# Performance work log

Measured on AMD Instinct MI355X. Metric: run time of the kernel, lower is better.

Reference implementation:

```python
import jax, jax.numpy as jnp
import numpy as np

VOCAB, HID = 32000, 1024
SEQ, BATCH = 64, 32

def setup_inputs() -> dict:
    key = jax.random.key(0)
    ks = jax.random.split(key, 12)
    w = 0.1  # winit uniform(-winit, winit)
    u = lambda k, shape: jax.random.uniform(k, shape, jnp.float32, -w, w)
    return {
        "x": jax.random.randint(ks[0], (SEQ, BATCH), 0, VOCAB),
        "emb_W": u(ks[1], (VOCAB, HID)),
        "Wx0": u(ks[2], (4 * HID, HID)), "Wh0": u(ks[3], (4 * HID, HID)),
        "bx0": u(ks[4], (4 * HID,)), "bh0": u(ks[5], (4 * HID,)),
        "Wx1": u(ks[6], (4 * HID, HID)), "Wh1": u(ks[7], (4 * HID, HID)),
        "bx1": u(ks[8], (4 * HID,)), "bh1": u(ks[9], (4 * HID,)),
        "fc_W": u(ks[10], (VOCAB, HID)), "fc_b": u(ks[11], (VOCAB,)),
        "h0": jnp.zeros((BATCH, HID), jnp.float32),
        "c0": jnp.zeros((BATCH, HID), jnp.float32),
        "h1": jnp.zeros((BATCH, HID), jnp.float32),
        "c1": jnp.zeros((BATCH, HID), jnp.float32),
    }

def _lstm_layer(inp, h, c, Wx, Wh, bx, bh):
    # inp: [T, B, H]; h, c: [B, H]
    def step(carry, x_t):
        h, c = carry
        gx = x_t @ Wx.T + bx      # [B, 4H]
        gh = h @ Wh.T + bh        # [B, 4H]
        xi, xf, xo, xn = jnp.split(gx, 4, axis=1)
        hi, hf, ho, hn = jnp.split(gh, 4, axis=1)
        i = jax.nn.sigmoid(xi + hi)
        f = jax.nn.sigmoid(xf + hf)
        o = jax.nn.sigmoid(xo + ho)
        n = jnp.tanh(xn + hn)
        c = f * c + i * n
        h = o * jnp.tanh(c)
        return (h, c), h
    (h, c), ys = jax.lax.scan(step, (h, c), inp)
    return ys, h, c

def reference(x, emb_W, Wx0, Wh0, bx0, bh0, Wx1, Wh1, bx1, bh1,
              fc_W, fc_b, h0, c0, h1, c1):
    e = emb_W[x]                                   # [T, B, H] embedding gather
    y0, h0f, c0f = _lstm_layer(e, h0, c0, Wx0, Wh0, bx0, bh0)
    y1, h1f, c1f = _lstm_layer(y0, h1, c1, Wx1, Wh1, bx1, bh1)
    # Linear.forward flattens to [T*B, H] then projects to vocab (dropout=0)
    logits = y1.reshape(-1, y1.shape[-1]) @ fc_W.T + fc_b  # [T*B, V]
    return logits, h0f, c0f, h1f, c1f
```

## Files before the change

kernel.cpp:

```cpp
#include <hip/hip_runtime.h>
#include <hip/hip_bf16.h>
#include <stdint.h>

typedef __bf16 bf16x8 __attribute__((ext_vector_type(8)));
typedef float  f32x4  __attribute__((ext_vector_type(4)));

#define HID   1024
#define SEQT  64
#define BATCH 32
#define GATES 4096
#define ROWS  2048
#define VOCAB 32000
#define HSLAB (64 * 32 * 16)
#define AGT __HIP_MEMORY_SCOPE_AGENT

__device__ __forceinline__ unsigned short f2bf(float f) {
    union { float f; unsigned u; } v; v.f = f;
    unsigned u = v.u + 0x7FFFu + ((v.u >> 16) & 1u);
    return (unsigned short)(u >> 16);
}

__device__ __forceinline__ float sigm(float x) { return 1.f / (1.f + expf(-x)); }

__device__ __forceinline__ void gload_lds16(const void* g, void* l) {
    __builtin_amdgcn_global_load_lds(
        (const __attribute__((address_space(1))) unsigned int*)g,
        (__attribute__((address_space(3))) unsigned int*)l,
        16, 0, 0);
}

__device__ __forceinline__ ushort4 cvt4(float4 v) {
    ushort4 o;
    o.x = f2bf(v.x); o.y = f2bf(v.y); o.z = f2bf(v.z); o.w = f2bf(v.w);
    return o;
}

__global__ __launch_bounds__(256) void prologue_k(
    const int* __restrict__ x, const float* __restrict__ embW,
    unsigned short* __restrict__ eb,
    const float* __restrict__ Wx0, unsigned short* __restrict__ Wx0b,
    const float* __restrict__ h0, const float* __restrict__ h1,
    unsigned short* __restrict__ h0b, unsigned short* __restrict__ h1b,
    int* __restrict__ bar)
{
    const int bid = blockIdx.x, tid = threadIdx.x;
    const float4* src = (const float4*)(embW + (size_t)x[bid] * HID);
    ((ushort4*)(eb + (size_t)bid * HID))[tid] = cvt4(src[tid]);
    int base = bid * 512 + tid;
    ((ushort4*)Wx0b)[base]       = cvt4(((const float4*)Wx0)[base]);
    ((ushort4*)Wx0b)[base + 256] = cvt4(((const float4*)Wx0)[base + 256]);
    int i = bid * 256 + tid;
    if (i < 32768) {
        int blk = i >> 9, b = (i >> 4) & 31, w = i & 15;
        int col = blk * 16 + w;
        h0b[i] = f2bf(h0[b * HID + col]);
        h1b[i] = f2bf(h1[b * HID + col]);
        if (i < 8192) bar[i] = 0;
    }
}

__global__ __launch_bounds__(256) void gemm_bt(
    const unsigned short* __restrict__ A,
    const unsigned short* __restrict__ B,
    float* __restrict__ C,
    const float* __restrict__ bias0,
    const float* __restrict__ bias1,
    int M, int N, int K)
{
    __shared__ unsigned short As[128][32];
    __shared__ unsigned short Bs[128][32];
    const int tid  = threadIdx.x;
    const int lane = tid & 63;
    const int wr   = (tid >> 7) & 1;
    const int wc   = (tid >> 6) & 1;

    const int nmp = M >> 7, nnp = N >> 7;
    const int nwg = nmp * nnp, per = nwg >> 3;
    const int wid = (blockIdx.x & 7) * per + (blockIdx.x >> 3);
    const int bm  = (wid % nmp) << 7;
    const int bn  = (wid / nmp) << 7;

    const int lr   = lane & 15;
    const int lk   = (lane >> 4) * 8;

    f32x4 acc[4][4];
    #pragma unroll
    for (int m = 0; m < 4; ++m)
        #pragma unroll
        for (int n = 0; n < 4; ++n) acc[m][n] = 0.f;

    for (int kt = 0; kt < K; kt += 32) {
        __syncthreads();
        #pragma unroll
        for (int i = 0; i < 2; ++i) {
            int ch = tid + i * 256;
            int r = ch >> 2, c8 = (ch & 3) * 8;
            gload_lds16(A + (size_t)(bm + r) * K + kt + c8, (char*)&As[0][0] + ch * 16);
            gload_lds16(B + (size_t)(bn + r) * K + kt + c8, (char*)&Bs[0][0] + ch * 16);
        }
        __syncthreads();
        bf16x8 af[4], bfr[4];
        #pragma unroll
        for (int m = 0; m < 4; ++m)
            af[m] = *(const bf16x8*)&As[wr * 64 + m * 16 + lr][lk];
        #pragma unroll
        for (int n = 0; n < 4; ++n)
            bfr[n] = *(const bf16x8*)&Bs[wc * 64 + n * 16 + lr][lk];
        #pragma unroll
        for (int m = 0; m < 4; ++m)
            #pragma unroll
            for (int n = 0; n < 4; ++n)
                acc[m][n] = __builtin_amdgcn_mfma_f32_16x16x32_bf16(af[m], bfr[n], acc[m][n], 0, 0, 0);
    }

    const int row0 = bm + wr * 64, col0 = bn + wc * 64;
    #pragma unroll
    for (int n = 0; n < 4; ++n) {
        int col = col0 + n * 16 + lr;
        float badd = 0.f;
        if (bias0) badd += bias0[col];
        if (bias1) badd += bias1[col];
        #pragma unroll
        for (int m = 0; m < 4; ++m) {
            #pragma unroll
            for (int j = 0; j < 4; ++j) {
                int row = row0 + m * 16 + (lane >> 4) * 4 + j;
                C[(size_t)row * N + col] = acc[m][n][j] + badd;
            }
        }
    }
}

__global__ __launch_bounds__(256, 1) void lstm_fused_k(
    const float* __restrict__ Wh0f,
    const float* __restrict__ Wx1f,
    const float* __restrict__ Wh1f,
    const float* __restrict__ gx0,
    const float* __restrict__ bx1,
    const float* __restrict__ bh1,
    const unsigned short* __restrict__ h0b,
    const unsigned short* __restrict__ h1b,
    const float* __restrict__ c0i,
    const float* __restrict__ c1i,
    unsigned short* __restrict__ y0x,
    unsigned short* __restrict__ y1x,
    float* __restrict__ part,
    float* __restrict__ h0f, float* __restrict__ c0f,
    float* __restrict__ h1f, float* __restrict__ c1f,
    int* __restrict__ bar,
    const float* __restrict__ fcW,
    unsigned short* __restrict__ fcWb)
{
    const int tid = threadIdx.x;
    const int bid = blockIdx.x;

    if (bid >= 192) {
        int base = (bid - 192) * 256 + tid;
        const float4* f4 = (const float4*)fcW;
        uint4* o4 = (uint4*)fcWb;
        const int n8 = VOCAB * HID / 8;
        for (int i = base; i < n8; i += 16384) {
            float4 v0 = f4[2 * i], v1 = f4[2 * i + 1];
            uint4 o;
            o.x = (unsigned)f2bf(v0.x) | ((unsigned)f2bf(v0.y) << 16);
            o.y = (unsigned)f2bf(v0.z) | ((unsigned)f2bf(v0.w) << 16);
            o.z = (unsigned)f2bf(v1.x) | ((unsigned)f2bf(v1.y) << 16);
            o.w = (unsigned)f2bf(v1.z) | ((unsigned)f2bf(v1.w) << 16);
            o4[i] = o;
        }
        return;
    }

    __builtin_amdgcn_fence(__ATOMIC_ACQUIRE, "agent");

    __shared__ char smem[65536 + 8192];
    float* pre = (float*)(smem + 65536);
    const int lane = tid & 63;
    const int wave = tid >> 6;
    const int role = bid >> 6;
    const int wg   = bid & 63;
    const int lr   = lane & 15;
    const int lk8  = (lane >> 4) * 8;
    const int r0   = lr, r1 = 16 + lr;
    const int kby  = (lane >> 4) * 16;
    const int eb_  = tid >> 3;
    const int ecp  = (tid & 7) * 2;
    const int ecol = wg * 16 + ecp;

    bf16x8 wf[32];
    {
        const float* Wsrc = (role == 0) ? Wh0f : (role == 1) ? Wx1f : Wh1f;
        const float* p = Wsrc + (size_t)(wave * HID + wg * 16 + lr) * HID + lk8;
        #pragma unroll
        for (int kk = 0; kk < 32; ++kk) {
            float4 v0 = *(const float4*)(p + kk * 32);
            float4 v1 = *(const float4*)(p + kk * 32 + 4);
            union { bf16x8 v; unsigned short s[8]; } u;
            u.s[0] = f2bf(v0.x); u.s[1] = f2bf(v0.y);
            u.s[2] = f2bf(v0.z); u.s[3] = f2bf(v0.w);
            u.s[4] = f2bf(v1.x); u.s[5] = f2bf(v1.y);
            u.s[6] = f2bf(v1.z); u.s[7] = f2bf(v1.w);
            wf[kk] = u.v;
        }
        #pragma unroll
        for (int kk = 0; kk < 32; ++kk) asm volatile("" : "+v"(wf[kk]));
    }

    auto stage_g = [&](const unsigned short* src) {
        #pragma unroll
        for (int j = 0; j < 16; ++j) {
            int base = wave * 16384 + j * 1024;
            int d = base + lane * 16;
            int r = d >> 11;
            int cb = (d & 2047) ^ ((r & 7) << 4);
            int e0 = cb >> 1;
            int g = (((e0 >> 4) * 32 + r) * 16 + (e0 & 15)) * 2;
            gload_lds16((const char*)src + g, smem + base);
        }
    };
    auto mm = [&](f32x4& A0, f32x4& A1) {
        #pragma unroll
        for (int kk = 0; kk < 32; ++kk) {
            int k2 = kk * 64 + kby;
            bf16x8 x0 = *(const bf16x8*)(smem + r0 * 2048 + (k2 ^ ((r0 & 7) << 4)));
            bf16x8 x1 = *(const bf16x8*)(smem + r1 * 2048 + (k2 ^ ((r1 & 7) << 4)));
            A0 = __builtin_amdgcn_mfma_f32_16x16x32_bf16(x0, wf[kk], A0, 0, 0, 0);
            A1 = __builtin_amdgcn_mfma_f32_16x16x32_bf16(x1, wf[kk], A1, 0, 0, 0);
        }
    };
    auto spill = [&](const f32x4& a0, const f32x4& a1) {
        float* pg = pre + wave * 512;
        #pragma unroll
        for (int j = 0; j < 4; ++j) {
            pg[((lane >> 4) * 4 + j) * 16 + lr]        = a0[j];
            pg[((lane >> 4) * 4 + j + 16) * 16 + lr]   = a1[j];
        }
    };
    auto pollge = [&](int grp, int val) {
        for (;;) {
            int f = __hip_atomic_load(&bar[(grp * 64 + lane) * 32],
                                      __ATOMIC_RELAXED, AGT);
            if (__all(f >= val)) break;
            __builtin_amdgcn_s_sleep(1);
        }
    };

    if (role == 0) {
        float creg0, creg1;
        { float2 c2 = *(const float2*)&c0i[eb_ * HID + ecol]; creg0 = c2.x; creg1 = c2.y; }
        for (int t = 0; t < SEQT; ++t) {
            float2 gpre[4];
            const float* gxr = gx0 + (size_t)(t * BATCH + eb_) * GATES + ecol;
            #pragma unroll
            for (int g = 0; g < 4; ++g) gpre[g] = *(const float2*)(gxr + g * HID);
            if (t > 0) pollge(0, t);
            asm volatile("" ::: "memory");
            stage_g(t == 0 ? h0b : y0x + (size_t)(t - 1) * HSLAB);
            __syncthreads();
            f32x4 a0 = 0.f, a1 = 0.f;
            mm(a0, a1);
            spill(a0, a1);
            __syncthreads();
            float2 P[4];
            #pragma unroll
            for (int g = 0; g < 4; ++g) {
                float2 pr = *(const float2*)&pre[(g * 32 + eb_) * 16 + ecp];
                P[g].x = pr.x + gpre[g].x; P[g].y = pr.y + gpre[g].y;
            }
            float i0 = sigm(P[0].x), fg0 = sigm(P[1].x), o0 = sigm(P[2].x), n0 = tanhf(P[3].x);
            float i1 = sigm(P[0].y), fg1 = sigm(P[1].y), o1 = sigm(P[2].y), n1 = tanhf(P[3].y);
            float cn0 = fg0 * creg0 + i0 * n0, cn1 = fg1 * creg1 + i1 * n1;
            float hv0 = o0 * tanhf(cn0), hv1 = o1 * tanhf(cn1);
            creg0 = cn0; creg1 = cn1;
            unsigned pk = (unsigned)f2bf(hv0) | ((unsigned)f2bf(hv1) << 16);
            __hip_atomic_store(
                (unsigned*)&y0x[(size_t)t * HSLAB + (wg * 32 + eb_) * 16 + ecp],
                pk, __ATOMIC_RELAXED, AGT);
            if (t == SEQT - 1) {
                *(float2*)&h0f[eb_ * HID + ecol] = make_float2(hv0, hv1);
                *(float2*)&c0f[eb_ * HID + ecol] = make_float2(cn0, cn1);
            }
            __syncthreads();
            if (tid == 0)
                __hip_atomic_store(&bar[wg * 32], t + 1, __ATOMIC_RELAXED, AGT);
        }
    } else if (role == 1) {
        for (int t = 0; t < SEQT; ++t) {
            pollge(0, t + 1);
            asm volatile("" ::: "memory");
            stage_g(y0x + (size_t)t * HSLAB);
            __syncthreads();
            f32x4 a0 = 0.f, a1 = 0.f;
            mm(a0, a1);
            {
                float* pb = part + (((size_t)(t * 4 + wave) * 64 + wg) * 32) * 16;
                int brow = (lane >> 4) * 4;
                #pragma unroll
                for (int j = 0; j < 4; ++j) {
                    __hip_atomic_store(pb + (brow + j) * 16 + lr,      a0[j],
                                       __ATOMIC_RELAXED, AGT);
                    __hip_atomic_store(pb + (brow + j + 16) * 16 + lr, a1[j],
                                       __ATOMIC_RELAXED, AGT);
                }
            }
            __syncthreads();
            if (tid == 0)
                __hip_atomic_store(&bar[(64 + wg) * 32], t + 1, __ATOMIC_RELAXED, AGT);
        }
    } else {
        float creg0, creg1;
        { float2 c2 = *(const float2*)&c1i[eb_ * HID + ecol]; creg0 = c2.x; creg1 = c2.y; }
        float2 b1r[4];
        #pragma unroll
        for (int g = 0; g < 4; ++g) {
            float2 a = *(const float2*)&bx1[g * HID + ecol];
            float2 b = *(const float2*)&bh1[g * HID + ecol];
            b1r[g].x = a.x + b.x; b1r[g].y = a.y + b.y;
        }
        for (int t = 0; t < SEQT; ++t) {
            pollge(1, t + 1);
            if (t > 0) pollge(2, t);
            asm volatile("" ::: "memory");
            stage_g(t == 0 ? h1b : y1x + (size_t)(t - 1) * HSLAB);
            __syncthreads();
            f32x4 a0 = 0.f, a1 = 0.f;
            mm(a0, a1);
            spill(a0, a1);
            __syncthreads();
            float2 P[4];
            #pragma unroll
            for (int g = 0; g < 4; ++g) {
                float2 pr = *(const float2*)&pre[(g * 32 + eb_) * 16 + ecp];
                float2 px = *(const float2*)(part +
                    ((((size_t)(t * 4 + g) * 64 + wg) * 32 + eb_) * 16 + ecp));
                P[g].x = pr.x + px.x + b1r[g].x;
                P[g].y = pr.y + px.y + b1r[g].y;
            }
            float i0 = sigm(P[0].x), fg0 = sigm(P[1].x), o0 = sigm(P[2].x), n0 = tanhf(P[3].x);
            float i1 = sigm(P[0].y), fg1 = sigm(P[1].y), o1 = sigm(P[2].y), n1 = tanhf(P[3].y);
            float cn0 = fg0 * creg0 + i0 * n0, cn1 = fg1 * creg1 + i1 * n1;
            float hv0 = o0 * tanhf(cn0), hv1 = o1 * tanhf(cn1);
            creg0 = cn0; creg1 = cn1;
            unsigned pk = (unsigned)f2bf(hv0) | ((unsigned)f2bf(hv1) << 16);
            __hip_atomic_store(
                (unsigned*)&y1x[(size_t)t * HSLAB + (wg * 32 + eb_) * 16 + ecp],
                pk, __ATOMIC_RELAXED, AGT);
            if (t == SEQT - 1) {
                *(float2*)&h1f[eb_ * HID + ecol] = make_float2(hv0, hv1);
                *(float2*)&c1f[eb_ * HID + ecol] = make_float2(cn0, cn1);
            }
            __syncthreads();
            if (tid == 0)
                __hip_atomic_store(&bar[(128 + wg) * 32], t + 1, __ATOMIC_RELAXED, AGT);
        }
    }
}

__global__ __launch_bounds__(512, 4) void fc_k(
    const unsigned short* __restrict__ y1x,
    const unsigned short* __restrict__ fcWb,
    const float* __restrict__ fcb,
    float* __restrict__ logits)
{
    __shared__ unsigned short As[256 * 32];
    __shared__ unsigned short Bs[128 * 32];
    const int tid  = threadIdx.x;
    const int lane = tid & 63;
    const int wave = tid >> 6;
    const int wr   = wave >> 1;
    const int wc   = wave & 1;
    const int lr   = lane & 15;
    const int lk   = (lane >> 4) * 8;

    const int per = 2000 >> 3;
    const int wid = ((int)blockIdx.x & 7) * per + ((int)blockIdx.x >> 3);
    const int bm  = (wid & 7) << 8;
    const int bn  = (wid >> 3) << 7;

    f32x4 acc[4][4];
    #pragma unroll
    for (int m = 0; m < 4; ++m)
        #pragma unroll
        for (int n = 0; n < 4; ++n) acc[m][n] = 0.f;

    for (int kt = 0; kt < HID; kt += 32) {
        __syncthreads();
        #pragma unroll
        for (int i = 0; i < 2; ++i) {
            int ch = tid + i * 512;
            int r = ch >> 2, c8 = (ch & 3) * 8;
            int R = bm + r, e = kt + c8;
            const char* asrc = (const char*)y1x +
                ((((size_t)(R >> 5) * 64 + (e >> 4)) * 32 + (R & 31)) * 16 + (e & 15)) * 2;
            gload_lds16(asrc, (char*)As + ch * 16);
        }
        {
            int r = tid >> 2, c8 = (tid & 3) * 8;
            gload_lds16(fcWb + (size_t)(bn + r) * HID + kt + c8, (char*)Bs + tid * 16);
        }
        __syncthreads();
        bf16x8 af[4], bfr[4];
        #pragma unroll
        for (int m = 0; m < 4; ++m)
            af[m] = *(const bf16x8*)&As[(wr * 64 + m * 16 + lr) * 32 + lk];
        #pragma unroll
        for (int n = 0; n < 4; ++n)
            bfr[n] = *(const bf16x8*)&Bs[(wc * 64 + n * 16 + lr) * 32 + lk];
        #pragma unroll
        for (int m = 0; m < 4; ++m)
            #pragma unroll
            for (int n = 0; n < 4; ++n)
                acc[m][n] = __builtin_amdgcn_mfma_f32_16x16x32_bf16(af[m], bfr[n], acc[m][n], 0, 0, 0);
    }

    const int row0 = bm + wr * 64, col0 = bn + wc * 64;
    #pragma unroll
    for (int n = 0; n < 4; ++n) {
        int col = col0 + n * 16 + lr;
        float badd = fcb[col];
        #pragma unroll
        for (int m = 0; m < 4; ++m) {
            #pragma unroll
            for (int j = 0; j < 4; ++j) {
                int row = row0 + m * 16 + (lane >> 4) * 4 + j;
                logits[(size_t)row * VOCAB + col] = acc[m][n][j] + badd;
            }
        }
    }
}

extern "C" void kernel_launch(void* const* d_in, const int* in_sizes, int n_in,
                              void* d_out, int out_size, void* d_ws, size_t ws_size,
                              hipStream_t stream) {
    const int*   x    = (const int*)d_in[0];
    const float* embW = (const float*)d_in[1];
    const float* Wx0  = (const float*)d_in[2];
    const float* Wh0  = (const float*)d_in[3];
    const float* bx0  = (const float*)d_in[4];
    const float* bh0  = (const float*)d_in[5];
    const float* Wx1  = (const float*)d_in[6];
    const float* Wh1  = (const float*)d_in[7];
    const float* bx1  = (const float*)d_in[8];
    const float* bh1  = (const float*)d_in[9];
    const float* fcW  = (const float*)d_in[10];
    const float* fcb  = (const float*)d_in[11];
    const float* h0   = (const float*)d_in[12];
    const float* c0   = (const float*)d_in[13];
    const float* h1   = (const float*)d_in[14];
    const float* c1   = (const float*)d_in[15];

    char* ws = (char*)d_ws;
    size_t off = 0;
    auto alloc = [&](size_t bytes) {
        char* p = ws + off;
        off += (bytes + 255) & ~(size_t)255;
        return p;
    };
    unsigned short* eb    = (unsigned short*)alloc((size_t)ROWS * HID * 2);
    unsigned short* Wx0b  = (unsigned short*)alloc((size_t)GATES * HID * 2);
    unsigned short* fcWb  = (unsigned short*)alloc((size_t)VOCAB * HID * 2);
    float*          gx0   = (float*)alloc((size_t)ROWS * GATES * 4);
    float*          part  = (float*)alloc((size_t)SEQT * 4 * 64 * 32 * 16 * 4);
    unsigned short* y0x   = (unsigned short*)alloc((size_t)SEQT * HSLAB * 2);
    unsigned short* y1x   = (unsigned short*)alloc((size_t)SEQT * HSLAB * 2);
    unsigned short* h0b   = (unsigned short*)alloc((size_t)BATCH * HID * 2);
    unsigned short* h1b   = (unsigned short*)alloc((size_t)BATCH * HID * 2);
    int*            bar   = (int*)alloc((size_t)256 * 32 * 4);
    (void)ws_size; (void)in_sizes; (void)n_in; (void)out_size;

    float* logits = (float*)d_out;
    float* h0f = logits + (size_t)ROWS * VOCAB;
    float* c0f = h0f + BATCH * HID;
    float* h1f = c0f + BATCH * HID;
    float* c1f = h1f + BATCH * HID;

    prologue_k<<<ROWS, 256, 0, stream>>>(x, embW, eb, Wx0, Wx0b,
                                         h0, h1, h0b, h1b, bar);
    gemm_bt<<<(ROWS / 128) * (GATES / 128), 256, 0, stream>>>(
        eb, Wx0b, gx0, bx0, bh0, ROWS, GATES, HID);
    lstm_fused_k<<<256, 256, 0, stream>>>(Wh0, Wx1, Wh1, gx0, bx1, bh1,
                                          h0b, h1b, c0, c1, y0x, y1x, part,
                                          h0f, c0f, h1f, c1f, bar, fcW, fcWb);
    fc_k<<<2000, 512, 0, stream>>>(y1x, fcWb, fcb, logits);
}
```

Measured before the change: 572.5 us.

## Replace flag barriers with NaN-sentinel polling on hidden-state slabs

Removes the per-step flag barriers and the LDS staging of hidden states. Consumers now read bf16 activations straight from global memory with atomic loads and spin until no word equals a NaN sentinel that the prologue writes into the y0/y1 buffers. Layer 1 now keeps both Wx1 and Wh1 in registers in one workgroup, which drops the separate Wx1 role and the partial-sum buffer and frees 64 blocks for the fcW conversion. This shortens the dependency chain per step, but it costs more register pressure, heavier global polling traffic, and it fails if a real hidden value ever equals the sentinel pattern.

```diff
diff --git a/kernel.cpp b/kernel.cpp
--- a/kernel.cpp
+++ b/kernel.cpp
@@ -12,6 +12,7 @@
 #define ROWS  2048
 #define VOCAB 32000
 #define HSLAB (64 * 32 * 16)
+#define SENTW 0x7FC07FC0u
 #define AGT __HIP_MEMORY_SCOPE_AGENT
 
 __device__ __forceinline__ unsigned short f2bf(float f) {
@@ -33,6 +34,13 @@
     ushort4 o;
     o.x = f2bf(v.x); o.y = f2bf(v.y); o.z = f2bf(v.z); o.w = f2bf(v.w);
     return o;
+}
+
+__device__ __forceinline__ unsigned long long aload(const void* p) {
+    return __hip_atomic_load((const unsigned long long*)p, __ATOMIC_RELAXED, AGT);
+}
+__device__ __forceinline__ int okw(unsigned long long q) {
+    return ((unsigned)q != SENTW) & ((unsigned)(q >> 32) != SENTW);
 }
 
 __global__ __launch_bounds__(256) void prologue_k(
@@ -41,7 +49,7 @@
     const float* __restrict__ Wx0, unsigned short* __restrict__ Wx0b,
     const float* __restrict__ h0, const float* __restrict__ h1,
     unsigned short* __restrict__ h0b, unsigned short* __restrict__ h1b,
-    int* __restrict__ bar)
+    uint4* __restrict__ y0x4, uint4* __restrict__ y1x4)
 {
     const int bid = blockIdx.x, tid = threadIdx.x;
     const float4* src = (const float4*)(embW + (size_t)x[bid] * HID);
@@ -55,8 +63,10 @@
         int col = blk * 16 + w;
         h0b[i] = f2bf(h0[b * HID + col]);
         h1b[i] = f2bf(h1[b * HID + col]);
-        if (i < 8192) bar[i] = 0;
-    }
+    }
+    uint4 s4; s4.x = s4.y = s4.z = s4.w = SENTW;
+    if (i < 262144) y0x4[i] = s4;
+    else            y1x4[i - 262144] = s4;
 }
 
 __global__ __launch_bounds__(256) void gemm_bt(
@@ -144,22 +154,20 @@
     const float* __restrict__ c1i,
     unsigned short* __restrict__ y0x,
     unsigned short* __restrict__ y1x,
-    float* __restrict__ part,
     float* __restrict__ h0f, float* __restrict__ c0f,
     float* __restrict__ h1f, float* __restrict__ c1f,
-    int* __restrict__ bar,
     const float* __restrict__ fcW,
     unsigned short* __restrict__ fcWb)
 {
     const int tid = threadIdx.x;
     const int bid = blockIdx.x;
 
-    if (bid >= 192) {
-        int base = (bid - 192) * 256 + tid;
+    if (bid >= 128) {
+        int base = (bid - 128) * 256 + tid;
         const float4* f4 = (const float4*)fcW;
         uint4* o4 = (uint4*)fcWb;
         const int n8 = VOCAB * HID / 8;
-        for (int i = base; i < n8; i += 16384) {
+        for (int i = base; i < n8; i += 32768) {
             float4 v0 = f4[2 * i], v1 = f4[2 * i + 1];
             uint4 o;
             o.x = (unsigned)f2bf(v0.x) | ((unsigned)f2bf(v0.y) << 16);
@@ -173,23 +181,22 @@
 
     __builtin_amdgcn_fence(__ATOMIC_ACQUIRE, "agent");
 
-    __shared__ char smem[65536 + 8192];
-    float* pre = (float*)(smem + 65536);
+    __shared__ char smem[90112];
+    float* pre = (float*)smem;
+
     const int lane = tid & 63;
     const int wave = tid >> 6;
     const int role = bid >> 6;
     const int wg   = bid & 63;
     const int lr   = lane & 15;
-    const int lk8  = (lane >> 4) * 8;
-    const int r0   = lr, r1 = 16 + lr;
-    const int kby  = (lane >> 4) * 16;
+    const int hi8  = lane >> 4;
+    const int lk8  = hi8 * 8;
     const int eb_  = tid >> 3;
     const int ecp  = (tid & 7) * 2;
     const int ecol = wg * 16 + ecp;
-
-    bf16x8 wf[32];
-    {
-        const float* Wsrc = (role == 0) ? Wh0f : (role == 1) ? Wx1f : Wh1f;
+    const int boff = (hi8 >> 1) * 1024 + (hi8 & 1) * 16;
+
+    auto ldw = [&](const float* Wsrc, bf16x8 (&W)[32]) {
         const float* p = Wsrc + (size_t)(wave * HID + wg * 16 + lr) * HID + lk8;
         #pragma unroll
         for (int kk = 0; kk < 32; ++kk) {
@@ -200,52 +207,58 @@
             u.s[2] = f2bf(v0.z); u.s[3] = f2bf(v0.w);
             u.s[4] = f2bf(v1.x); u.s[5] = f2bf(v1.y);
             u.s[6] = f2bf(v1.z); u.s[7] = f2bf(v1.w);
-            wf[kk] = u.v;
-        }
-        #pragma unroll
-        for (int kk = 0; kk < 32; ++kk) asm volatile("" : "+v"(wf[kk]));
-    }
-
-    auto stage_g = [&](const unsigned short* src) {
-        #pragma unroll
-        for (int j = 0; j < 16; ++j) {
-            int base = wave * 16384 + j * 1024;
-            int d = base + lane * 16;
-            int r = d >> 11;
-            int cb = (d & 2047) ^ ((r & 7) << 4);
-            int e0 = cb >> 1;
-            int g = (((e0 >> 4) * 32 + r) * 16 + (e0 & 15)) * 2;
-            gload_lds16((const char*)src + g, smem + base);
-        }
+            W[kk] = u.v;
+        }
+        #pragma unroll
+        for (int kk = 0; kk < 32; ++kk) asm volatile("" : "+v"(W[kk]));
     };
-    auto mm = [&](f32x4& A0, f32x4& A1) {
+
+    auto mmf = [&](const unsigned short* slab, const bf16x8 (&W)[32],
+                   f32x4& A0, f32x4& A1) {
+        const char* p0 = (const char*)slab + boff + lr * 32;
+        const char* p1 = p0 + 512;
+        union FR { bf16x8 v; unsigned long long q[2]; };
+        FR f0[8], f1[8];
+        #pragma unroll
+        for (int i = 0; i < 8; ++i) {
+            f0[i].q[0] = aload(p0 + i * 2048); f0[i].q[1] = aload(p0 + i * 2048 + 8);
+            f1[i].q[0] = aload(p1 + i * 2048); f1[i].q[1] = aload(p1 + i * 2048 + 8);
+        }
         #pragma unroll
         for (int kk = 0; kk < 32; ++kk) {
-            int k2 = kk * 64 + kby;
-            bf16x8 x0 = *(const bf16x8*)(smem + r0 * 2048 + (k2 ^ ((r0 & 7) << 4)));
-            bf16x8 x1 = *(const bf16x8*)(smem + r1 * 2048 + (k2 ^ ((r1 & 7) << 4)));
-            A0 = __builtin_amdgcn_mfma_f32_16x16x32_bf16(x0, wf[kk], A0, 0, 0, 0);
-            A1 = __builtin_amdgcn_mfma_f32_16x16x32_bf16(x1, wf[kk], A1, 0, 0, 0);
+            const int s = kk & 7;
+            for (;;) {
+                int ok = okw(f0[s].q[0]) & okw(f0[s].q[1]) &
+                         okw(f1[s].q[0]) & okw(f1[s].q[1]);
+                if (__all(ok)) break;
+                if (!okw(f0[s].q[0])) f0[s].q[0] = aload(p0 + kk * 2048);
+                if (!okw(f0[s].q[1])) f0[s].q[1] = aload(p0 + kk * 2048 + 8);
+                if (!okw(f1[s].q[0])) f1[s].q[0] = aload(p1 + kk * 2048);
+                if (!okw(f1[s].q[1])) f1[s].q[1] = aload(p1 + kk * 2048 + 8);
+            }
+            A0 = __builtin_amdgcn_mfma_f32_16x16x32_bf16(f0[s].v, W[kk], A0, 0, 0, 0);
+            A1 = __builtin_amdgcn_mfma_f32_16x16x32_bf16(f1[s].v, W[kk], A1, 0, 0, 0);
+            if (kk < 24) {
+                f0[s].q[0] = aload(p0 + (kk + 8) * 2048);
+                f0[s].q[1] = aload(p0 + (kk + 8) * 2048 + 8);
+                f1[s].q[0] = aload(p1 + (kk + 8) * 2048);
+                f1[s].q[1] = aload(p1 + (kk + 8) * 2048 + 8);
+            }
         }
     };
+
     auto spill = [&](const f32x4& a0, const f32x4& a1) {
         float* pg = pre + wave * 512;
         #pragma unroll
         for (int j = 0; j < 4; ++j) {
-            pg[((lane >> 4) * 4 + j) * 16 + lr]        = a0[j];
-            pg[((lane >> 4) * 4 + j + 16) * 16 + lr]   = a1[j];
+            pg[(hi8 * 4 + j) * 16 + lr]      = a0[j];
+            pg[(hi8 * 4 + j + 16) * 16 + lr] = a1[j];
         }
     };
-    auto pollge = [&](int grp, int val) {
-        for (;;) {
-            int f = __hip_atomic_load(&bar[(grp * 64 + lane) * 32],
-                                      __ATOMIC_RELAXED, AGT);
-            if (__all(f >= val)) break;
-            __builtin_amdgcn_s_sleep(1);
-        }
-    };
 
     if (role == 0) {
+        bf16x8 wf[32];
+        ldw(Wh0f, wf);
         float creg0, creg1;
         { float2 c2 = *(const float2*)&c0i[eb_ * HID + ecol]; creg0 = c2.x; creg1 = c2.y; }
         for (int t = 0; t < SEQT; ++t) {
@@ -253,12 +266,8 @@
             const float* gxr = gx0 + (size_t)(t * BATCH + eb_) * GATES + ecol;
             #pragma unroll
             for (int g = 0; g < 4; ++g) gpre[g] = *(const float2*)(gxr + g * HID);
-            if (t > 0) pollge(0, t);
-            asm volatile("" ::: "memory");
-            stage_g(t == 0 ? h0b : y0x + (size_t)(t - 1) * HSLAB);
-            __syncthreads();
             f32x4 a0 = 0.f, a1 = 0.f;
-            mm(a0, a1);
+            mmf(t == 0 ? h0b : y0x + (size_t)(t - 1) * HSLAB, wf, a0, a1);
             spill(a0, a1);
             __syncthreads();
             float2 P[4];
@@ -280,34 +289,11 @@
                 *(float2*)&h0f[eb_ * HID + ecol] = make_float2(hv0, hv1);
                 *(float2*)&c0f[eb_ * HID + ecol] = make_float2(cn0, cn1);
             }
-            __syncthreads();
-            if (tid == 0)
-                __hip_atomic_store(&bar[wg * 32], t + 1, __ATOMIC_RELAXED, AGT);
-        }
-    } else if (role == 1) {
-        for (int t = 0; t < SEQT; ++t) {
-            pollge(0, t + 1);
-            asm volatile("" ::: "memory");
-            stage_g(y0x + (size_t)t * HSLAB);
-            __syncthreads();
-            f32x4 a0 = 0.f, a1 = 0.f;
-            mm(a0, a1);
-            {
-                float* pb = part + (((size_t)(t * 4 + wave) * 64 + wg) * 32) * 16;
-                int brow = (lane >> 4) * 4;
-                #pragma unroll
-                for (int j = 0; j < 4; ++j) {
-                    __hip_atomic_store(pb + (brow + j) * 16 + lr,      a0[j],
-                                       __ATOMIC_RELAXED, AGT);
-                    __hip_atomic_store(pb + (brow + j + 16) * 16 + lr, a1[j],
-                                       __ATOMIC_RELAXED, AGT);
-                }
-            }
-            __syncthreads();
-            if (tid == 0)
-                __hip_atomic_store(&bar[(64 + wg) * 32], t + 1, __ATOMIC_RELAXED, AGT);
         }
     } else {
+        bf16x8 wx[32], wh[32];
+        ldw(Wx1f, wx);
+        ldw(Wh1f, wh);
         float creg0, creg1;
         { float2 c2 = *(const float2*)&c1i[eb_ * HID + ecol]; creg0 = c2.x; creg1 = c2.y; }
         float2 b1r[4];
@@ -318,23 +304,17 @@
             b1r[g].x = a.x + b.x; b1r[g].y = a.y + b.y;
         }
         for (int t = 0; t < SEQT; ++t) {
-            pollge(1, t + 1);
-            if (t > 0) pollge(2, t);
-            asm volatile("" ::: "memory");
-            stage_g(t == 0 ? h1b : y1x + (size_t)(t - 1) * HSLAB);
-            __syncthreads();
             f32x4 a0 = 0.f, a1 = 0.f;
-            mm(a0, a1);
+            mmf(y0x + (size_t)t * HSLAB, wx, a0, a1);
+            mmf(t == 0 ? h1b : y1x + (size_t)(t - 1) * HSLAB, wh, a0, a1);
             spill(a0, a1);
             __syncthreads();
             float2 P[4];
             #pragma unroll
             for (int g = 0; g < 4; ++g) {
                 float2 pr = *(const float2*)&pre[(g * 32 + eb_) * 16 + ecp];
-                float2 px = *(const float2*)(part +
-                    ((((size_t)(t * 4 + g) * 64 + wg) * 32 + eb_) * 16 + ecp));
-                P[g].x = pr.x + px.x + b1r[g].x;
-                P[g].y = pr.y + px.y + b1r[g].y;
+                P[g].x = pr.x + b1r[g].x;
+                P[g].y = pr.y + b1r[g].y;
             }
             float i0 = sigm(P[0].x), fg0 = sigm(P[1].x), o0 = sigm(P[2].x), n0 = tanhf(P[3].x);
             float i1 = sigm(P[0].y), fg1 = sigm(P[1].y), o1 = sigm(P[2].y), n1 = tanhf(P[3].y);
@@ -349,9 +329,6 @@
                 *(float2*)&h1f[eb_ * HID + ecol] = make_float2(hv0, hv1);
                 *(float2*)&c1f[eb_ * HID + ecol] = make_float2(cn0, cn1);
             }
-            __syncthreads();
-            if (tid == 0)
-                __hip_atomic_store(&bar[(128 + wg) * 32], t + 1, __ATOMIC_RELAXED, AGT);
         }
     }
 }
@@ -460,12 +437,10 @@
     unsigned short* Wx0b  = (unsigned short*)alloc((size_t)GATES * HID * 2);
     unsigned short* fcWb  = (unsigned short*)alloc((size_t)VOCAB * HID * 2);
     float*          gx0   = (float*)alloc((size_t)ROWS * GATES * 4);
-    float*          part  = (float*)alloc((size_t)SEQT * 4 * 64 * 32 * 16 * 4);
     unsigned short* y0x   = (unsigned short*)alloc((size_t)SEQT * HSLAB * 2);
     unsigned short* y1x   = (unsigned short*)alloc((size_t)SEQT * HSLAB * 2);
     unsigned short* h0b   = (unsigned short*)alloc((size_t)BATCH * HID * 2);
     unsigned short* h1b   = (unsigned short*)alloc((size_t)BATCH * HID * 2);
-    int*            bar   = (int*)alloc((size_t)256 * 32 * 4);
     (void)ws_size; (void)in_sizes; (void)n_in; (void)out_size;
 
     float* logits = (float*)d_out;
@@ -475,11 +450,12 @@
     float* c1f = h1f + BATCH * HID;
 
     prologue_k<<<ROWS, 256, 0, stream>>>(x, embW, eb, Wx0, Wx0b,
-                                         h0, h1, h0b, h1b, bar);
+                                         h0, h1, h0b, h1b,
+                                         (uint4*)y0x, (uint4*)y1x);
     gemm_bt<<<(ROWS / 128) * (GATES / 128), 256, 0, stream>>>(
         eb, Wx0b, gx0, bx0, bh0, ROWS, GATES, HID);
     lstm_fused_k<<<256, 256, 0, stream>>>(Wh0, Wx1, Wh1, gx0, bx1, bh1,
-                                          h0b, h1b, c0, c1, y0x, y1x, part,
-                                          h0f, c0f, h1f, c1f, bar, fcW, fcWb);
+                                          h0b, h1b, c0, c1, y0x, y1x,
+                                          h0f, c0f, h1f, c1f, fcW, fcWb);
     fc_k<<<2000, 512, 0, stream>>>(y1x, fcWb, fcb, logits);
 }
```

After: 1.658 ms. 190% more time.

## Overlap first vocab panels of FC projection with LSTM recurrence via flag polling

Applied to the files above, without the earlier changes.

The 64 spare blocks of the fused LSTM kernel previously only converted fcW to bf16. They now convert one assigned 128-column panel of fcW and then compute that panel's logits for 128-row chunks as soon as the layer-1 LSTM has published enough timesteps, which they detect by polling the step barrier. The hidden-state staging layout changes from a tiled layout to a row-major XOR-swizzled layout, so LDS staging becomes a plain contiguous copy. The trailing fc_k launch shrinks to cover only the remaining vocab columns. The aim is to hide FC work behind the serial recurrence. The trade-off is that these blocks stall waiting on LSTM progress and could contend with the recurrent blocks.

```diff
diff --git a/kernel.cpp b/kernel.cpp
--- a/kernel.cpp
+++ b/kernel.cpp
@@ -51,10 +51,10 @@
     ((ushort4*)Wx0b)[base + 256] = cvt4(((const float4*)Wx0)[base + 256]);
     int i = bid * 256 + tid;
     if (i < 32768) {
-        int blk = i >> 9, b = (i >> 4) & 31, w = i & 15;
-        int col = blk * 16 + w;
-        h0b[i] = f2bf(h0[b * HID + col]);
-        h1b[i] = f2bf(h1[b * HID + col]);
+        int b = i >> 10, col = i & 1023;
+        int dst = b * 1024 + (col ^ ((b & 7) << 3));
+        h0b[dst] = f2bf(h0[i]);
+        h1b[dst] = f2bf(h1[i]);
         if (i < 8192) bar[i] = 0;
     }
 }
@@ -149,33 +149,105 @@
     float* __restrict__ h1f, float* __restrict__ c1f,
     int* __restrict__ bar,
     const float* __restrict__ fcW,
-    unsigned short* __restrict__ fcWb)
+    unsigned short* __restrict__ fcWb,
+    const float* __restrict__ fcb,
+    float* __restrict__ logits)
 {
-    const int tid = threadIdx.x;
-    const int bid = blockIdx.x;
-
-    if (bid >= 192) {
-        int base = (bid - 192) * 256 + tid;
-        const float4* f4 = (const float4*)fcW;
-        uint4* o4 = (uint4*)fcWb;
-        const int n8 = VOCAB * HID / 8;
-        for (int i = base; i < n8; i += 16384) {
-            float4 v0 = f4[2 * i], v1 = f4[2 * i + 1];
-            uint4 o;
-            o.x = (unsigned)f2bf(v0.x) | ((unsigned)f2bf(v0.y) << 16);
-            o.y = (unsigned)f2bf(v0.z) | ((unsigned)f2bf(v0.w) << 16);
-            o.z = (unsigned)f2bf(v1.x) | ((unsigned)f2bf(v1.y) << 16);
-            o.w = (unsigned)f2bf(v1.z) | ((unsigned)f2bf(v1.w) << 16);
-            o4[i] = o;
-        }
-        return;
-    }
+    const int tid  = threadIdx.x;
+    const int bid  = blockIdx.x;
+    const int lane = tid & 63;
 
     __builtin_amdgcn_fence(__ATOMIC_ACQUIRE, "agent");
 
     __shared__ char smem[65536 + 8192];
     float* pre = (float*)(smem + 65536);
-    const int lane = tid & 63;
+
+    auto pollge = [&](int grp, int val) {
+        for (;;) {
+            int f = __hip_atomic_load(&bar[(grp * 64 + lane) * 32],
+                                      __ATOMIC_RELAXED, AGT);
+            if (__all(f >= val)) break;
+            __builtin_amdgcn_s_sleep(1);
+        }
+    };
+
+    if (bid >= 192) {
+        const int p = bid - 192;
+        auto cvtpanel = [&](int q) {
+            const float4* f4 = (const float4*)(fcW + (size_t)q * 128 * HID);
+            uint4* o4 = (uint4*)(fcWb + (size_t)q * 128 * HID);
+            for (int i = tid; i < 128 * HID / 8; i += 256) {
+                float4 v0 = f4[2 * i], v1 = f4[2 * i + 1];
+                uint4 o;
+                o.x = (unsigned)f2bf(v0.x) | ((unsigned)f2bf(v0.y) << 16);
+                o.y = (unsigned)f2bf(v0.z) | ((unsigned)f2bf(v0.w) << 16);
+                o.z = (unsigned)f2bf(v1.x) | ((unsigned)f2bf(v1.y) << 16);
+                o.w = (unsigned)f2bf(v1.z) | ((unsigned)f2bf(v1.w) << 16);
+                o4[i] = o;
+            }
+        };
+        cvtpanel(p);
+        for (int q = 64 + p; q < 250; q += 64) cvtpanel(q);
+        __syncthreads();
+
+        const int wr = (tid >> 7) & 1, wc = (tid >> 6) & 1;
+        const int lr = lane & 15, lk = (lane >> 4) * 8;
+        unsigned short* As = (unsigned short*)smem;
+        unsigned short* Bs = (unsigned short*)smem + 4096;
+        for (int m = 0; m < 16; ++m) {
+            pollge(2, 4 * m + 4);
+            asm volatile("" ::: "memory");
+            f32x4 acc[4][4];
+            #pragma unroll
+            for (int mi = 0; mi < 4; ++mi)
+                #pragma unroll
+                for (int ni = 0; ni < 4; ++ni) acc[mi][ni] = 0.f;
+            for (int kt = 0; kt < HID; kt += 32) {
+                __syncthreads();
+                #pragma unroll
+                for (int i = 0; i < 2; ++i) {
+                    int ch = tid + i * 256;
+                    int r = ch >> 2, c8 = (ch & 3) * 8;
+                    int R = m * 128 + r, e = kt + c8;
+                    const char* asrc = (const char*)y1x + ((size_t)(R >> 5) << 16)
+                        + (R & 31) * 2048 + ((e * 2) ^ ((R & 7) << 4));
+                    gload_lds16(asrc, (char*)As + ch * 16);
+                    gload_lds16(fcWb + (size_t)(p * 128 + r) * HID + e,
+                                (char*)Bs + ch * 16);
+                }
+                __syncthreads();
+                bf16x8 af[4], bfr[4];
+                #pragma unroll
+                for (int mi = 0; mi < 4; ++mi)
+                    af[mi] = *(const bf16x8*)&As[(wr * 64 + mi * 16 + lr) * 32 + lk];
+                #pragma unroll
+                for (int ni = 0; ni < 4; ++ni)
+                    bfr[ni] = *(const bf16x8*)&Bs[(wc * 64 + ni * 16 + lr) * 32 + lk];
+                #pragma unroll
+                for (int mi = 0; mi < 4; ++mi)
+                    #pragma unroll
+                    for (int ni = 0; ni < 4; ++ni)
+                        acc[mi][ni] = __builtin_amdgcn_mfma_f32_16x16x32_bf16(
+                            af[mi], bfr[ni], acc[mi][ni], 0, 0, 0);
+            }
+            const int row0 = m * 128 + wr * 64, col0 = p * 128 + wc * 64;
+            #pragma unroll
+            for (int ni = 0; ni < 4; ++ni) {
+                int col = col0 + ni * 16 + lr;
+                float badd = fcb[col];
+                #pragma unroll
+                for (int mi = 0; mi < 4; ++mi) {
+                    #pragma unroll
+                    for (int j = 0; j < 4; ++j) {
+                        int row = row0 + mi * 16 + (lane >> 4) * 4 + j;
+                        logits[(size_t)row * VOCAB + col] = acc[mi][ni][j] + badd;
+                    }
+                }
+            }
+        }
+        return;
+    }
+
     const int wave = tid >> 6;
     const int role = bid >> 6;
     const int wg   = bid & 63;
@@ -210,12 +282,7 @@
         #pragma unroll
         for (int j = 0; j < 16; ++j) {
             int base = wave * 16384 + j * 1024;
-            int d = base + lane * 16;
-            int r = d >> 11;
-            int cb = (d & 2047) ^ ((r & 7) << 4);
-            int e0 = cb >> 1;
-            int g = (((e0 >> 4) * 32 + r) * 16 + (e0 & 15)) * 2;
-            gload_lds16((const char*)src + g, smem + base);
+            gload_lds16((const char*)src + base + lane * 16, smem + base);
         }
     };
     auto mm = [&](f32x4& A0, f32x4& A1) {
@@ -236,14 +303,7 @@
             pg[((lane >> 4) * 4 + j + 16) * 16 + lr]   = a1[j];
         }
     };
-    auto pollge = [&](int grp, int val) {
-        for (;;) {
-            int f = __hip_atomic_load(&bar[(grp * 64 + lane) * 32],
-                                      __ATOMIC_RELAXED, AGT);
-            if (__all(f >= val)) break;
-            __builtin_amdgcn_s_sleep(1);
-        }
-    };
+    const unsigned pboff = (unsigned)(eb_ * 2048 + ((ecol * 2) ^ ((eb_ & 7) << 4)));
 
     if (role == 0) {
         float creg0, creg1;
@@ -274,7 +334,7 @@
             creg0 = cn0; creg1 = cn1;
             unsigned pk = (unsigned)f2bf(hv0) | ((unsigned)f2bf(hv1) << 16);
             __hip_atomic_store(
-                (unsigned*)&y0x[(size_t)t * HSLAB + (wg * 32 + eb_) * 16 + ecp],
+                (unsigned*)((char*)y0x + (size_t)t * 65536 + pboff),
                 pk, __ATOMIC_RELAXED, AGT);
             if (t == SEQT - 1) {
                 *(float2*)&h0f[eb_ * HID + ecol] = make_float2(hv0, hv1);
@@ -343,7 +403,7 @@
             creg0 = cn0; creg1 = cn1;
             unsigned pk = (unsigned)f2bf(hv0) | ((unsigned)f2bf(hv1) << 16);
             __hip_atomic_store(
-                (unsigned*)&y1x[(size_t)t * HSLAB + (wg * 32 + eb_) * 16 + ecp],
+                (unsigned*)((char*)y1x + (size_t)t * 65536 + pboff),
                 pk, __ATOMIC_RELAXED, AGT);
             if (t == SEQT - 1) {
                 *(float2*)&h1f[eb_ * HID + ecol] = make_float2(hv0, hv1);
@@ -372,10 +432,10 @@
     const int lr   = lane & 15;
     const int lk   = (lane >> 4) * 8;
 
-    const int per = 2000 >> 3;
+    const int per = 1488 >> 3;
     const int wid = ((int)blockIdx.x & 7) * per + ((int)blockIdx.x >> 3);
     const int bm  = (wid & 7) << 8;
-    const int bn  = (wid >> 3) << 7;
+    const int bn  = ((wid >> 3) + 64) << 7;
 
     f32x4 acc[4][4];
     #pragma unroll
@@ -390,8 +450,8 @@
             int ch = tid + i * 512;
             int r = ch >> 2, c8 = (ch & 3) * 8;
             int R = bm + r, e = kt + c8;
-            const char* asrc = (const char*)y1x +
-                ((((size_t)(R >> 5) * 64 + (e >> 4)) * 32 + (R & 31)) * 16 + (e & 15)) * 2;
+            const char* asrc = (const char*)y1x + ((size_t)(R >> 5) << 16)
+                + (R & 31) * 2048 + ((e * 2) ^ ((R & 7) << 4));
             gload_lds16(asrc, (char*)As + ch * 16);
         }
         {
@@ -480,6 +540,7 @@
         eb, Wx0b, gx0, bx0, bh0, ROWS, GATES, HID);
     lstm_fused_k<<<256, 256, 0, stream>>>(Wh0, Wx1, Wh1, gx0, bx1, bh1,
                                           h0b, h1b, c0, c1, y0x, y1x, part,
-                                          h0f, c0f, h1f, c1f, bar, fcW, fcWb);
-    fc_k<<<2000, 512, 0, stream>>>(y1x, fcWb, fcb, logits);
-}
+                                          h0f, c0f, h1f, c1f, bar, fcW, fcWb,
+                                          fcb, logits);
+    fc_k<<<1488, 512, 0, stream>>>(y1x, fcWb, fcb, logits);
+}
```

Result: slower. 624.8 us (+9.1%).
